# Kernel tuning notes

Hardware: AMD Instinct MI355X
Metric: run time of the kernel (lower is better)

## Reference

```python
import jax, jax.numpy as jnp
import numpy as np

H, C = 4, 128          # heads, hidden_channels
HC = H * C             # 512
F_IN = 9               # node_feat_dim
G_DIM = 50             # global_feat_dim (20 + 30 MACCS)
N = 30000              # nodes
E = 240000             # edges (before self-loops)
B = 64                 # graphs
EPS_BN = 1e-5
SLOPE = 0.2            # GATv2 LeakyReLU negative slope


def _glorot(key, shape):
    fan_in, fan_out = shape[0], shape[-1]
    lim = (6.0 / (fan_in + fan_out)) ** 0.5
    return jax.random.uniform(key, shape, jnp.float32, -lim, lim)


def setup_inputs() -> dict:
    key = jax.random.key(0)
    ks = jax.random.split(key, 20)
    x = jax.random.normal(ks[0], (N, F_IN), jnp.float32)
    global_feat = jax.random.normal(ks[1], (B, G_DIM), jnp.float32)
    edge_index = jax.random.randint(ks[2], (2, E), 0, N, jnp.int64) if jax.config.jax_enable_x64 else jax.random.randint(ks[2], (2, E), 0, N, jnp.int32)
    batch = jnp.sort(jax.random.randint(ks[3], (N,), 0, B, edge_index.dtype))
    return {
        "x": x, "global_feat": global_feat,
        # GATv2 layer 1
        "W1l": _glorot(ks[4], (F_IN, HC)), "b1l": jnp.zeros((HC,), jnp.float32),
        "W1r": _glorot(ks[5], (F_IN, HC)), "b1r": jnp.zeros((HC,), jnp.float32),
        "att1": _glorot(ks[6], (1, H, C))[0], "bias1": jnp.zeros((HC,), jnp.float32),
        # GATv2 layer 2
        "W2l": _glorot(ks[7], (HC, HC)), "b2l": jnp.zeros((HC,), jnp.float32),
        "W2r": _glorot(ks[8], (HC, HC)), "b2r": jnp.zeros((HC,), jnp.float32),
        "att2": _glorot(ks[9], (1, H, C))[0], "bias2": jnp.zeros((HC,), jnp.float32),
        # BatchNorms
        "bn1_g": jnp.ones((HC,), jnp.float32), "bn1_b": jnp.zeros((HC,), jnp.float32),
        "bn2_g": jnp.ones((HC,), jnp.float32), "bn2_b": jnp.zeros((HC,), jnp.float32),
        # MLP head
        "fc1_w": _glorot(ks[10], (HC + G_DIM, C)), "fc1_b": jnp.zeros((C,), jnp.float32),
        "fc2_w": _glorot(ks[11], (C, 1)), "fc2_b": jnp.zeros((1,), jnp.float32),
        "edge_index": edge_index, "batch": batch,
    }


def gatv2_layer(x, src, dst, Wl, bl, Wr, br, att, bias):
    n = x.shape[0]
    xl = (x @ Wl + bl).reshape(n, H, C)   # source transform
    xr = (x @ Wr + br).reshape(n, H, C)   # target transform
    m = xl[src] + xr[dst]                 # [E, H, C] gathered messages
    e = jnp.sum(jax.nn.leaky_relu(m, SLOPE) * att, axis=-1)  # [E, H]
    # segment softmax over edges grouped by target node
    e_max = jax.ops.segment_max(e, dst, num_segments=n)
    p = jnp.exp(e - e_max[dst])
    denom = jax.ops.segment_sum(p, dst, num_segments=n)
    alpha = p / (denom[dst] + 1e-16)      # [E, H]
    out = jax.ops.segment_sum(alpha[:, :, None] * xl[src], dst, num_segments=n)
    return out.reshape(n, HC) + bias


def batchnorm(x, g, b):
    mu = jnp.mean(x, axis=0)
    var = jnp.mean((x - mu) ** 2, axis=0)  # biased var (torch BN train mode)
    return (x - mu) * jax.lax.rsqrt(var + EPS_BN) * g + b


def reference(x, global_feat, W1l, b1l, W1r, b1r, att1, bias1,
              W2l, b2l, W2r, b2r, att2, bias2,
              bn1_g, bn1_b, bn2_g, bn2_b,
              fc1_w, fc1_b, fc2_w, fc2_b, edge_index, batch):
    n = x.shape[0]
    # add self-loops (PyG GATv2 default)
    loops = jnp.arange(n, dtype=edge_index.dtype)
    src = jnp.concatenate([edge_index[0], loops])
    dst = jnp.concatenate([edge_index[1], loops])

    h = gatv2_layer(x, src, dst, W1l, b1l, W1r, b1r, att1, bias1)
    h = jax.nn.relu(batchnorm(h, bn1_g, bn1_b))
    h = gatv2_layer(h, src, dst, W2l, b2l, W2r, b2r, att2, bias2)
    h = jax.nn.relu(batchnorm(h, bn2_g, bn2_b))

    # global mean pool over graphs
    sums = jax.ops.segment_sum(h, batch, num_segments=B)
    counts = jax.ops.segment_sum(jnp.ones((n, 1), h.dtype), batch, num_segments=B)
    pooled = sums / jnp.maximum(counts, 1.0)

    z = jnp.concatenate([pooled, global_feat], axis=1)
    z = jax.nn.relu(z @ fc1_w + fc1_b)  # dropout is identity in eval
    return jnp.squeeze(z @ fc2_w + fc2_b, axis=-1)
```

## Files before the change

### kernel.cpp

```cpp
#include <hip/hip_runtime.h>
#include <math.h>

#define NHEAD 4
#define CCH 128
#define HCD 512
#define SLOPE 0.2f
#define EPS_BN 1e-5f
#define PSPLIT 8

typedef short s8v __attribute__((ext_vector_type(8)));
typedef float f32x4 __attribute__((ext_vector_type(4)));

__device__ __forceinline__ unsigned short f2bf(float f) {
    unsigned int u = __float_as_uint(f);
    return (unsigned short)((u + 0x7FFFu + ((u >> 16) & 1u)) >> 16);
}
__device__ __forceinline__ float bf2f(unsigned short b) {
    return __uint_as_float(((unsigned int)b) << 16);
}

__global__ void lin1_kernel(const float* __restrict__ x,
                            const float* __restrict__ Wl, const float* __restrict__ bl,
                            const float* __restrict__ Wr, const float* __restrict__ br,
                            float* __restrict__ xl, float* __restrict__ xr, int n) {
    int gid = blockIdx.x * blockDim.x + threadIdx.x;
    if (gid >= n * HCD) return;
    int node = gid >> 9;
    int c = gid & (HCD - 1);
    const float* xrow = x + node * 9;
    float a = bl[c], bz = br[c];
#pragma unroll
    for (int k = 0; k < 9; ++k) {
        float xv = xrow[k];
        a  = fmaf(xv, Wl[k * HCD + c], a);
        bz = fmaf(xv, Wr[k * HCD + c], bz);
    }
    xl[gid] = a;
    xr[gid] = bz;
}

__global__ void splitA_kernel(const float* __restrict__ h,
                              const float* __restrict__ scale, const float* __restrict__ shift,
                              unsigned short* __restrict__ Ah, unsigned short* __restrict__ Al,
                              int total4) {
    int gid = blockIdx.x * blockDim.x + threadIdx.x;
    if (gid >= total4) return;
    int c4 = gid & 127;
    float4 v = ((const float4*)h)[gid];
    float4 sc = ((const float4*)scale)[c4];
    float4 sh = ((const float4*)shift)[c4];
    float f0 = fmaxf(fmaf(v.x, sc.x, sh.x), 0.f);
    float f1 = fmaxf(fmaf(v.y, sc.y, sh.y), 0.f);
    float f2 = fmaxf(fmaf(v.z, sc.z, sh.z), 0.f);
    float f3 = fmaxf(fmaf(v.w, sc.w, sh.w), 0.f);
    unsigned short h0 = f2bf(f0), h1 = f2bf(f1), h2 = f2bf(f2), h3 = f2bf(f3);
    short4 hv = make_short4((short)h0, (short)h1, (short)h2, (short)h3);
    short4 lv = make_short4((short)f2bf(f0 - bf2f(h0)), (short)f2bf(f1 - bf2f(h1)),
                            (short)f2bf(f2 - bf2f(h2)), (short)f2bf(f3 - bf2f(h3)));
    ((short4*)Ah)[gid] = hv;
    ((short4*)Al)[gid] = lv;
}

__global__ void splitBT_kernel(const float* __restrict__ Wl, const float* __restrict__ Wr,
                               unsigned short* __restrict__ BThl, unsigned short* __restrict__ BTll,
                               unsigned short* __restrict__ BThr, unsigned short* __restrict__ BTlr) {
    int gid = blockIdx.x * blockDim.x + threadIdx.x;
    int col = gid >> 9;
    int k = gid & 511;
    float vl = Wl[k * HCD + col];
    float vr = Wr[k * HCD + col];
    unsigned short hl = f2bf(vl);
    unsigned short hr = f2bf(vr);
    BThl[gid] = hl; BTll[gid] = f2bf(vl - bf2f(hl));
    BThr[gid] = hr; BTlr[gid] = f2bf(vr - bf2f(hr));
}

__global__ __launch_bounds__(256) void gemm_mfma_kernel(
        const unsigned short* __restrict__ Ah, const unsigned short* __restrict__ Al,
        const unsigned short* __restrict__ BThL, const unsigned short* __restrict__ BTlL,
        const unsigned short* __restrict__ BThR, const unsigned short* __restrict__ BTlR,
        const float* __restrict__ biasl, const float* __restrict__ biasr,
        float* __restrict__ outL, float* __restrict__ outR, int M) {
    __shared__ short sAh[2][4096], sAl[2][4096], sBh[2][4096], sBl[2][4096];
    const int nrt = gridDim.x >> 3;
    const int bphys = blockIdx.x;
    const int l = (bphys & 7) * nrt + (bphys >> 3);
    const int y = l & 7;
    const int row0 = (l >> 3) * 128;
    const unsigned short* BTh = (y < 4) ? BThL : BThR;
    const unsigned short* BTl = (y < 4) ? BTlL : BTlR;
    const float* bias = (y < 4) ? biasl : biasr;
    float* C = (y < 4) ? outL : outR;
    const int col0 = (y & 3) * 128;
    const int tid  = threadIdx.x;
    const int wave = tid >> 6;
    const int lane = tid & 63;
    const int str = tid >> 2;
    const int skb = tid & 3;

    f32x4 acc[4][4];
#pragma unroll
    for (int i = 0; i < 4; ++i)
#pragma unroll
        for (int j = 0; j < 4; ++j) acc[i][j] = (f32x4){0.f, 0.f, 0.f, 0.f};

    const int abase = (wave & 1) * 2048;
    const int bbase = (wave >> 1) * 2048;
    const int rkb = lane >> 4;
    const int rrow = (lane & 15) ^ (rkb << 1);
    const int roff = rkb * 128 + rrow * 8;

    s8v pAh[2], pAl[2], pBh[2], pBl[2];
    const s8v zero8 = (s8v){0,0,0,0,0,0,0,0};

#define GLOAD(k0)                                                                     \
    {                                                                                 \
        _Pragma("unroll")                                                             \
        for (int cc = 0; cc < 2; ++cc) {                                              \
            int r = str + cc * 64;                                                    \
            if (row0 + r < M) {                                                       \
                pAh[cc] = *(const s8v*)(Ah + (size_t)(row0 + r) * 512 + (k0) + skb * 8); \
                pAl[cc] = *(const s8v*)(Al + (size_t)(row0 + r) * 512 + (k0) + skb * 8); \
            } else { pAh[cc] = zero8; pAl[cc] = zero8; }                              \
            pBh[cc] = *(const s8v*)(BTh + (size_t)(col0 + r) * 512 + (k0) + skb * 8); \
            pBl[cc] = *(const s8v*)(BTl + (size_t)(col0 + r) * 512 + (k0) + skb * 8); \
        }                                                                             \
    }

#define LSTORE(buf)                                                                   \
    {                                                                                 \
        _Pragma("unroll")                                                             \
        for (int cc = 0; cc < 2; ++cc) {                                              \
            int r = str + cc * 64;                                                    \
            int idx = (r >> 4) * 512 + skb * 128 + (((r & 15) ^ (skb << 1)) * 8);     \
            *(s8v*)&sAh[buf][idx] = pAh[cc];                                          \
            *(s8v*)&sAl[buf][idx] = pAl[cc];                                          \
            *(s8v*)&sBh[buf][idx] = pBh[cc];                                          \
            *(s8v*)&sBl[buf][idx] = pBl[cc];                                          \
        }                                                                             \
    }

    GLOAD(0);
    LSTORE(0);
    GLOAD(32);
    __syncthreads();

    for (int k0 = 0; k0 < 512; k0 += 32) {
        const int cur = (k0 >> 5) & 1;
#pragma unroll
        for (int sr = 0; sr < 4; ++sr) {
            s8v ah = *(const s8v*)&sAh[cur][abase + sr * 512 + roff];
            s8v al = *(const s8v*)&sAl[cur][abase + sr * 512 + roff];
#pragma unroll
            for (int sc = 0; sc < 4; ++sc) {
                s8v bh = *(const s8v*)&sBh[cur][bbase + sc * 512 + roff];
                s8v bl = *(const s8v*)&sBl[cur][bbase + sc * 512 + roff];
                acc[sr][sc] = __builtin_amdgcn_mfma_f32_16x16x32_bf16(ah, bh, acc[sr][sc], 0, 0, 0);
                acc[sr][sc] = __builtin_amdgcn_mfma_f32_16x16x32_bf16(al, bh, acc[sr][sc], 0, 0, 0);
                acc[sr][sc] = __builtin_amdgcn_mfma_f32_16x16x32_bf16(ah, bl, acc[sr][sc], 0, 0, 0);
            }
        }
        if (k0 + 32 < 512) {
            LSTORE(cur ^ 1);
            if (k0 + 64 < 512) GLOAD(k0 + 64);
            __syncthreads();
        }
    }
#undef GLOAD
#undef LSTORE
    const int crow = row0 + (wave & 1) * 64;
    const int ccol = col0 + (wave >> 1) * 64;
#pragma unroll
    for (int sr = 0; sr < 4; ++sr) {
        int rbase = crow + sr * 16 + ((lane >> 4) << 2);
#pragma unroll
        for (int sc = 0; sc < 4; ++sc) {
            int col = ccol + sc * 16 + (lane & 15);
            float bb = bias[col];
#pragma unroll
            for (int j = 0; j < 4; ++j) {
                int r = rbase + j;
                if (r < M) C[(size_t)r * 512 + col] = acc[sr][sc][j] + bb;
            }
        }
    }
}


__global__ void hist_kernel(const int* __restrict__ edst, int* __restrict__ deg, int E, int Etot) {
    int e = blockIdx.x * blockDim.x + threadIdx.x;
    if (e >= Etot) return;
    int dst = (e < E) ? edst[e] : (e - E);
    atomicAdd(&deg[dst], 1);
}

__global__ __launch_bounds__(1024) void scan_kernel(const int* __restrict__ deg,
                                                    int* __restrict__ rowstart, int n) {
    __shared__ int buf[1024];
    __shared__ int carry;
    if (threadIdx.x == 0) carry = 0;
    __syncthreads();
    for (int base = 0; base < n; base += 1024) {
        int i = base + (int)threadIdx.x;
        int v = (i < n) ? deg[i] : 0;
        buf[threadIdx.x] = v;
        __syncthreads();
        for (int off = 1; off < 1024; off <<= 1) {
            int t = (threadIdx.x >= (unsigned)off) ? buf[threadIdx.x - off] : 0;
            __syncthreads();
            buf[threadIdx.x] += t;
            __syncthreads();
        }
        if (i < n) rowstart[i] = carry + buf[threadIdx.x] - v;
        int blocksum = buf[1023];
        __syncthreads();
        if (threadIdx.x == 0) carry += blocksum;
        __syncthreads();
    }
    if (threadIdx.x == 0) rowstart[n] = carry;
}

__global__ void scatter_kernel(const int* __restrict__ esrc, const int* __restrict__ edst,
                               const int* __restrict__ rowstart, int* __restrict__ cursor,
                               int* __restrict__ s_src, int E, int Etot) {
    int e = blockIdx.x * blockDim.x + threadIdx.x;
    if (e >= Etot) return;
    int src = (e < E) ? esrc[e] : (e - E);
    int dst = (e < E) ? edst[e] : (e - E);
    int pos = rowstart[dst] + atomicAdd(&cursor[dst], 1);
    s_src[pos] = src;
}

__global__ __launch_bounds__(256) void gat_fused_kernel(
        const float* __restrict__ xl, const float* __restrict__ xr,
        const float* __restrict__ att,
        const int* __restrict__ rowstart, const int* __restrict__ s_src,
        float* __restrict__ out) {
    int node = blockIdx.x;
    int h    = threadIdx.x >> 6;
    int lane = threadIdx.x & 63;
    int beg = rowstart[node];
    int end = rowstart[node + 1];
    int c0 = h * CCH + (lane << 1);
    float2 r2 = *(const float2*)(xr + (size_t)node * HCD + c0);
    float2 a2 = *(const float2*)(att + c0);
    float m = -3.0e38f, den = 0.f, acc0 = 0.f, acc1 = 0.f;

    int j = beg;
    float2 q0, q1, q2, q3;
    q0 = *(const float2*)(xl + (size_t)s_src[j] * HCD + c0);
    if (j + 1 < end) q1 = *(const float2*)(xl + (size_t)s_src[j + 1] * HCD + c0);
    if (j + 2 < end) q2 = *(const float2*)(xl + (size_t)s_src[j + 2] * HCD + c0);
    if (j + 3 < end) q3 = *(const float2*)(xl + (size_t)s_src[j + 3] * HCD + c0);

    while (j + 1 < end) {
        float2 A = q0, B = q1;
        q0 = q2; q1 = q3;
        if (j + 4 < end) q2 = *(const float2*)(xl + (size_t)s_src[j + 4] * HCD + c0);
        if (j + 5 < end) q3 = *(const float2*)(xl + (size_t)s_src[j + 5] * HCD + c0);
        float ta0 = A.x + r2.x; ta0 = (ta0 > 0.f) ? ta0 : SLOPE * ta0;
        float ta1 = A.y + r2.y; ta1 = (ta1 > 0.f) ? ta1 : SLOPE * ta1;
        float tb0 = B.x + r2.x; tb0 = (tb0 > 0.f) ? tb0 : SLOPE * tb0;
        float tb1 = B.y + r2.y; tb1 = (tb1 > 0.f) ? tb1 : SLOPE * tb1;
        float sA = fmaf(ta0, a2.x, ta1 * a2.y);
        float sB = fmaf(tb0, a2.x, tb1 * a2.y);
#pragma unroll
        for (int k = 1; k < 64; k <<= 1) {
            sA += __shfl_xor(sA, k);
            sB += __shfl_xor(sB, k);
        }
        float mn = fmaxf(m, fmaxf(sA, sB));
        float sc = expf(m - mn);
        float pA = expf(sA - mn);
        float pB = expf(sB - mn);
        den  = fmaf(den,  sc, pA + pB);
        acc0 = fmaf(acc0, sc, fmaf(pA, A.x, pB * B.x));
        acc1 = fmaf(acc1, sc, fmaf(pA, A.y, pB * B.y));
        m = mn;
        j += 2;
    }
    if (j < end) {
        float2 A = q0;
        float ta0 = A.x + r2.x; ta0 = (ta0 > 0.f) ? ta0 : SLOPE * ta0;
        float ta1 = A.y + r2.y; ta1 = (ta1 > 0.f) ? ta1 : SLOPE * ta1;
        float sA = fmaf(ta0, a2.x, ta1 * a2.y);
#pragma unroll
        for (int k = 1; k < 64; k <<= 1) sA += __shfl_xor(sA, k);
        float mn = fmaxf(m, sA);
        float sc = expf(m - mn);
        float pA = expf(sA - mn);
        den  = fmaf(den,  sc, pA);
        acc0 = fmaf(acc0, sc, pA * A.x);
        acc1 = fmaf(acc1, sc, pA * A.y);
    }
    float inv = 1.0f / (den + 1e-16f);
    *(float2*)(out + (size_t)node * HCD + c0) = make_float2(acc0 * inv, acc1 * inv);
}

__global__ void bn_stats_kernel(const float* __restrict__ h, float* __restrict__ sum,
                                float* __restrict__ sumsq, int n) {
    int c = blockIdx.y * blockDim.x + threadIdx.x;
    int r0 = blockIdx.x * 128;
    int r1 = min(r0 + 128, n);
    float s = 0.f, s2 = 0.f;
    for (int r = r0; r < r1; ++r) {
        float v = h[(size_t)r * HCD + c];
        s += v;
        s2 = fmaf(v, v, s2);
    }
    atomicAdd(&sum[c], s);
    atomicAdd(&sumsq[c], s2);
}

__global__ void bn_finalize_kernel(const float* __restrict__ sum, const float* __restrict__ sumsq,
                                   const float* __restrict__ g, const float* __restrict__ b,
                                   float* __restrict__ scale, float* __restrict__ shift, int n) {
    int c = threadIdx.x;
    float inv_n = 1.0f / (float)n;
    float mu = sum[c] * inv_n;
    float var = fmaxf(sumsq[c] * inv_n - mu * mu, 0.0f);
    float sc = g[c] * rsqrtf(var + EPS_BN);
    scale[c] = sc;
    shift[c] = b[c] - mu * sc;
}

__device__ __forceinline__ int lower_bound_i(const int* __restrict__ a, int n, int key) {
    int lo = 0, hi = n;
    while (lo < hi) {
        int mid = (lo + hi) >> 1;
        if (a[mid] < key) lo = mid + 1; else hi = mid;
    }
    return lo;
}

__global__ void pool_partial_kernel(const float* __restrict__ h, const int* __restrict__ batch,
                                    const float* __restrict__ scale, const float* __restrict__ shift,
                                    float* __restrict__ pooled, int n) {
    int g = blockIdx.x;
    int chunk = blockIdx.y;
    int c = threadIdx.x;
    int start = lower_bound_i(batch, n, g);
    int end   = lower_bound_i(batch, n, g + 1);
    int len = end - start;
    int cs = start + (int)(((long long)len * chunk) / PSPLIT);
    int ce = start + (int)(((long long)len * (chunk + 1)) / PSPLIT);
    if (cs >= ce) return;
    float sc = scale[c], sh = shift[c];
    float s = 0.f;
    for (int r = cs; r < ce; ++r)
        s += fmaxf(fmaf(h[(size_t)r * HCD + c], sc, sh), 0.f);
    atomicAdd(&pooled[(size_t)g * HCD + c], s);
}

__global__ void head_kernel(const float* __restrict__ pooled, const float* __restrict__ gfeat,
                            const int* __restrict__ batch,
                            const float* __restrict__ fc1w, const float* __restrict__ fc1b,
                            const float* __restrict__ fc2w, const float* __restrict__ fc2b,
                            float* __restrict__ out, int gdim, int n) {
    int g = blockIdx.x;
    int j = threadIdx.x;
    int start = lower_bound_i(batch, n, g);
    int end   = lower_bound_i(batch, n, g + 1);
    float icnt = 1.0f / (float)max(end - start, 1);
    float acc = fc1b[j];
    const float* prow = pooled + (size_t)g * HCD;
    for (int i = 0; i < HCD; ++i) acc = fmaf(prow[i] * icnt, fc1w[i * CCH + j], acc);
    const float* grow = gfeat + (size_t)g * gdim;
    for (int i = 0; i < gdim; ++i) acc = fmaf(grow[i], fc1w[(HCD + i) * CCH + j], acc);
    acc = fmaxf(acc, 0.f);
    __shared__ float z[CCH];
    z[j] = acc * fc2w[j];
    __syncthreads();
    for (int s = CCH / 2; s > 0; s >>= 1) {
        if (j < s) z[j] += z[j + s];
        __syncthreads();
    }
    if (j == 0) out[g] = z[0] + fc2b[0];
}

extern "C" void kernel_launch(void* const* d_in, const int* in_sizes, int n_in,
                              void* d_out, int out_size, void* d_ws, size_t ws_size,
                              hipStream_t stream) {
    const float* x     = (const float*)d_in[0];
    const float* gfeat = (const float*)d_in[1];
    const float* W1l   = (const float*)d_in[2];
    const float* b1l   = (const float*)d_in[3];
    const float* W1r   = (const float*)d_in[4];
    const float* b1r   = (const float*)d_in[5];
    const float* att1  = (const float*)d_in[6];
    const float* W2l   = (const float*)d_in[8];
    const float* b2l   = (const float*)d_in[9];
    const float* W2r   = (const float*)d_in[10];
    const float* b2r   = (const float*)d_in[11];
    const float* att2  = (const float*)d_in[12];
    const float* bn1_g = (const float*)d_in[14];
    const float* bn1_b = (const float*)d_in[15];
    const float* bn2_g = (const float*)d_in[16];
    const float* bn2_b = (const float*)d_in[17];
    const float* fc1w  = (const float*)d_in[18];
    const float* fc1b  = (const float*)d_in[19];
    const float* fc2w  = (const float*)d_in[20];
    const float* fc2b  = (const float*)d_in[21];
    const int* eidx    = (const int*)d_in[22];
    const int* batch   = (const int*)d_in[23];

    const int n    = in_sizes[0] / 9;
    const int E    = in_sizes[22] / 2;
    const int Etot = E + n;
    const int b    = out_size;
    const int gdim = in_sizes[1] / b;
    const int* esrc = eidx;
    const int* edst = eidx + E;

    float* ws = (float*)d_ws;
    size_t nHC = (size_t)n * HCD;
    float* xl      = ws;
    float* xr      = xl + nHC;
    float* hbuf    = xr + nHC;
    int* deg       = (int*)(hbuf + nHC);
    int* rowstart  = deg + n;
    int* cursor    = rowstart + n + 1;
    int* s_src     = cursor + n;
    float* bnsum   = (float*)(s_src + Etot);
    float* bnsumsq = bnsum + HCD;
    float* bnscale = bnsumsq + HCD;
    float* bnshift = bnscale + HCD;
    float* pooled  = bnshift + HCD;
    unsigned short* Ah   = (unsigned short*)(pooled + (size_t)b * HCD);
    unsigned short* Al   = Ah + nHC;
    unsigned short* BThl = Al + nHC;
    unsigned short* BTll = BThl + HCD * HCD;
    unsigned short* BThr = BTll + HCD * HCD;
    unsigned short* BTlr = BThr + HCD * HCD;

    const int BLK = 256;
    const int linBlocks  = (int)((nHC + BLK - 1) / BLK);
    const int eBlocks    = (Etot + BLK - 1) / BLK;
    const int bnxBlocks  = (n + 127) / 128;
    const int saBlocks   = (int)((nHC / 4 + BLK - 1) / BLK);
    const int nrt        = (n + 127) / 128;
    dim3 gemmGrid(nrt * 8);

    hipMemsetAsync(deg, 0, (size_t)(2 * n + 1) * sizeof(int), stream);
    hipMemsetAsync(cursor, 0, (size_t)n * sizeof(int), stream);
    hist_kernel<<<eBlocks, BLK, 0, stream>>>(edst, deg, E, Etot);
    scan_kernel<<<1, 1024, 0, stream>>>(deg, rowstart, n);
    scatter_kernel<<<eBlocks, BLK, 0, stream>>>(esrc, edst, rowstart, cursor, s_src, E, Etot);
    splitBT_kernel<<<(HCD * HCD) / BLK, BLK, 0, stream>>>(W2l, W2r, BThl, BTll, BThr, BTlr);

    lin1_kernel<<<linBlocks, BLK, 0, stream>>>(x, W1l, b1l, W1r, b1r, xl, xr, n);
    gat_fused_kernel<<<n, 256, 0, stream>>>(xl, xr, att1, rowstart, s_src, hbuf);
    hipMemsetAsync(bnsum, 0, HCD * 2 * sizeof(float), stream);
    bn_stats_kernel<<<dim3(bnxBlocks, 2), BLK, 0, stream>>>(hbuf, bnsum, bnsumsq, n);
    bn_finalize_kernel<<<1, HCD, 0, stream>>>(bnsum, bnsumsq, bn1_g, bn1_b, bnscale, bnshift, n);

    splitA_kernel<<<saBlocks, BLK, 0, stream>>>(hbuf, bnscale, bnshift, Ah, Al, (int)(nHC / 4));
    gemm_mfma_kernel<<<gemmGrid, BLK, 0, stream>>>(Ah, Al, BThl, BTll, BThr, BTlr,
                                                   b2l, b2r, xl, xr, n);
    gat_fused_kernel<<<n, 256, 0, stream>>>(xl, xr, att2, rowstart, s_src, hbuf);
    hipMemsetAsync(bnsum, 0, HCD * 2 * sizeof(float), stream);
    bn_stats_kernel<<<dim3(bnxBlocks, 2), BLK, 0, stream>>>(hbuf, bnsum, bnsumsq, n);
    bn_finalize_kernel<<<1, HCD, 0, stream>>>(bnsum, bnsumsq, bn2_g, bn2_b, bnscale, bnshift, n);

    hipMemsetAsync(pooled, 0, (size_t)b * HCD * sizeof(float), stream);
    pool_partial_kernel<<<dim3(b, PSPLIT), HCD, 0, stream>>>(hbuf, batch, bnscale, bnshift, pooled, n);
    head_kernel<<<b, CCH, 0, stream>>>(pooled, gfeat, batch, fc1w, fc1b, fc2w, fc2b,
                                       (float*)d_out, gdim, n);
}
```

Baseline: 775.8 us.

## Parallelize CSR scan across blocks and map one wavefront per GAT node

```diff
diff --git a/kernel.cpp b/kernel.cpp
--- a/kernel.cpp
+++ b/kernel.cpp
@@ -194,30 +194,43 @@
     atomicAdd(&deg[dst], 1);
 }
 
-__global__ __launch_bounds__(1024) void scan_kernel(const int* __restrict__ deg,
-                                                    int* __restrict__ rowstart, int n) {
+__global__ void scan1_kernel(const int* __restrict__ deg, int* __restrict__ rowstart,
+                             int* __restrict__ bsum, int n) {
+    __shared__ int buf[256];
+    int i = blockIdx.x * 256 + (int)threadIdx.x;
+    int v = (i < n) ? deg[i] : 0;
+    buf[threadIdx.x] = v;
+    __syncthreads();
+    for (int off = 1; off < 256; off <<= 1) {
+        int t = (threadIdx.x >= (unsigned)off) ? buf[threadIdx.x - off] : 0;
+        __syncthreads();
+        buf[threadIdx.x] += t;
+        __syncthreads();
+    }
+    if (i < n) rowstart[i] = buf[threadIdx.x] - v;
+    if (threadIdx.x == 255) bsum[blockIdx.x] = buf[255];
+}
+
+__global__ __launch_bounds__(1024) void scan2_kernel(int* __restrict__ bsum,
+                                                     int* __restrict__ boff,
+                                                     int nb, int* __restrict__ total_out) {
     __shared__ int buf[1024];
-    __shared__ int carry;
-    if (threadIdx.x == 0) carry = 0;
+    int v = ((int)threadIdx.x < nb) ? bsum[threadIdx.x] : 0;
+    buf[threadIdx.x] = v;
     __syncthreads();
-    for (int base = 0; base < n; base += 1024) {
-        int i = base + (int)threadIdx.x;
-        int v = (i < n) ? deg[i] : 0;
-        buf[threadIdx.x] = v;
+    for (int off = 1; off < 1024; off <<= 1) {
+        int t = (threadIdx.x >= (unsigned)off) ? buf[threadIdx.x - off] : 0;
         __syncthreads();
-        for (int off = 1; off < 1024; off <<= 1) {
-            int t = (threadIdx.x >= (unsigned)off) ? buf[threadIdx.x - off] : 0;
-            __syncthreads();
-            buf[threadIdx.x] += t;
-            __syncthreads();
-        }
-        if (i < n) rowstart[i] = carry + buf[threadIdx.x] - v;
-        int blocksum = buf[1023];
+        buf[threadIdx.x] += t;
         __syncthreads();
-        if (threadIdx.x == 0) carry += blocksum;
-        __syncthreads();
-    }
-    if (threadIdx.x == 0) rowstart[n] = carry;
+    }
+    if ((int)threadIdx.x < nb) boff[threadIdx.x] = buf[threadIdx.x] - v;
+    if (threadIdx.x == 1023) *total_out = buf[1023];
+}
+
+__global__ void scan3_kernel(int* __restrict__ rowstart, const int* __restrict__ boff, int n) {
+    int i = blockIdx.x * 256 + (int)threadIdx.x;
+    if (i < n) rowstart[i] += boff[blockIdx.x];
 }
 
 __global__ void scatter_kernel(const int* __restrict__ esrc, const int* __restrict__ edst,
@@ -235,37 +248,70 @@
         const float* __restrict__ xl, const float* __restrict__ xr,
         const float* __restrict__ att,
         const int* __restrict__ rowstart, const int* __restrict__ s_src,
-        float* __restrict__ out) {
-    int node = blockIdx.x;
-    int h    = threadIdx.x >> 6;
+        float* __restrict__ out, int n) {
+    int node = blockIdx.x * 4 + (int)(threadIdx.x >> 6);
+    if (node >= n) return;
     int lane = threadIdx.x & 63;
+    int c0 = lane << 3;
+    const float4* xr4 = (const float4*)(xr + (size_t)node * HCD + c0);
+    float4 r0 = xr4[0], r1 = xr4[1];
+    const float4* at4 = (const float4*)(att + c0);
+    float4 a0 = at4[0], a1 = at4[1];
     int beg = rowstart[node];
     int end = rowstart[node + 1];
-    int c0 = h * CCH + (lane << 1);
-    float2 r2 = *(const float2*)(xr + (size_t)node * HCD + c0);
-    float2 a2 = *(const float2*)(att + c0);
-    float m = -3.0e38f, den = 0.f, acc0 = 0.f, acc1 = 0.f;
+    float m = -3.0e38f, den = 0.f;
+    float4 acc0 = make_float4(0.f, 0.f, 0.f, 0.f);
+    float4 acc1 = make_float4(0.f, 0.f, 0.f, 0.f);
+
+#define SCORE(s, X0, X1)                                                       \
+    {                                                                          \
+        float t;                                                               \
+        s = 0.f;                                                               \
+        t = X0.x + r0.x; t = (t > 0.f) ? t : SLOPE * t; s = fmaf(t, a0.x, s);  \
+        t = X0.y + r0.y; t = (t > 0.f) ? t : SLOPE * t; s = fmaf(t, a0.y, s);  \
+        t = X0.z + r0.z; t = (t > 0.f) ? t : SLOPE * t; s = fmaf(t, a0.z, s);  \
+        t = X0.w + r0.w; t = (t > 0.f) ? t : SLOPE * t; s = fmaf(t, a0.w, s);  \
+        t = X1.x + r1.x; t = (t > 0.f) ? t : SLOPE * t; s = fmaf(t, a1.x, s);  \
+        t = X1.y + r1.y; t = (t > 0.f) ? t : SLOPE * t; s = fmaf(t, a1.y, s);  \
+        t = X1.z + r1.z; t = (t > 0.f) ? t : SLOPE * t; s = fmaf(t, a1.z, s);  \
+        t = X1.w + r1.w; t = (t > 0.f) ? t : SLOPE * t; s = fmaf(t, a1.w, s);  \
+    }
 
     int j = beg;
-    float2 q0, q1, q2, q3;
-    q0 = *(const float2*)(xl + (size_t)s_src[j] * HCD + c0);
-    if (j + 1 < end) q1 = *(const float2*)(xl + (size_t)s_src[j + 1] * HCD + c0);
-    if (j + 2 < end) q2 = *(const float2*)(xl + (size_t)s_src[j + 2] * HCD + c0);
-    if (j + 3 < end) q3 = *(const float2*)(xl + (size_t)s_src[j + 3] * HCD + c0);
+    float4 qa0, qa1, qb0, qb1, qc0, qc1, qd0, qd1;
+    {
+        const float4* p = (const float4*)(xl + (size_t)s_src[j] * HCD + c0);
+        qa0 = p[0]; qa1 = p[1];
+    }
+    if (j + 1 < end) {
+        const float4* p = (const float4*)(xl + (size_t)s_src[j + 1] * HCD + c0);
+        qb0 = p[0]; qb1 = p[1];
+    }
+    if (j + 2 < end) {
+        const float4* p = (const float4*)(xl + (size_t)s_src[j + 2] * HCD + c0);
+        qc0 = p[0]; qc1 = p[1];
+    }
+    if (j + 3 < end) {
+        const float4* p = (const float4*)(xl + (size_t)s_src[j + 3] * HCD + c0);
+        qd0 = p[0]; qd1 = p[1];
+    }
 
     while (j + 1 < end) {
-        float2 A = q0, B = q1;
-        q0 = q2; q1 = q3;
-        if (j + 4 < end) q2 = *(const float2*)(xl + (size_t)s_src[j + 4] * HCD + c0);
-        if (j + 5 < end) q3 = *(const float2*)(xl + (size_t)s_src[j + 5] * HCD + c0);
-        float ta0 = A.x + r2.x; ta0 = (ta0 > 0.f) ? ta0 : SLOPE * ta0;
-        float ta1 = A.y + r2.y; ta1 = (ta1 > 0.f) ? ta1 : SLOPE * ta1;
-        float tb0 = B.x + r2.x; tb0 = (tb0 > 0.f) ? tb0 : SLOPE * tb0;
-        float tb1 = B.y + r2.y; tb1 = (tb1 > 0.f) ? tb1 : SLOPE * tb1;
-        float sA = fmaf(ta0, a2.x, ta1 * a2.y);
-        float sB = fmaf(tb0, a2.x, tb1 * a2.y);
-#pragma unroll
-        for (int k = 1; k < 64; k <<= 1) {
+        float4 A0 = qa0, A1 = qa1, B0 = qb0, B1 = qb1;
+        qa0 = qc0; qa1 = qc1; qb0 = qd0; qb1 = qd1;
+        if (j + 4 < end) {
+            const float4* p = (const float4*)(xl + (size_t)s_src[j + 4] * HCD + c0);
+            qc0 = p[0]; qc1 = p[1];
+        }
+        if (j + 5 < end) {
+            const float4* p = (const float4*)(xl + (size_t)s_src[j + 5] * HCD + c0);
+            qd0 = p[0]; qd1 = p[1];
+        }
+        float sA, sB;
+        SCORE(sA, A0, A1);
+        SCORE(sB, B0, B1);
+#pragma unroll
+        for (int k = 1; k < 16; k <<= 1) {
             sA += __shfl_xor(sA, k);
             sB += __shfl_xor(sB, k);
         }
@@ -273,28 +319,42 @@
         float sc = expf(m - mn);
         float pA = expf(sA - mn);
         float pB = expf(sB - mn);
-        den  = fmaf(den,  sc, pA + pB);
-        acc0 = fmaf(acc0, sc, fmaf(pA, A.x, pB * B.x));
-        acc1 = fmaf(acc1, sc, fmaf(pA, A.y, pB * B.y));
+        den = fmaf(den, sc, pA + pB);
+        acc0.x = fmaf(acc0.x, sc, fmaf(pA, A0.x, pB * B0.x));
+        acc0.y = fmaf(acc0.y, sc, fmaf(pA, A0.y, pB * B0.y));
+        acc0.z = fmaf(acc0.z, sc, fmaf(pA, A0.z, pB * B0.z));
+        acc0.w = fmaf(acc0.w, sc, fmaf(pA, A0.w, pB * B0.w));
+        acc1.x = fmaf(acc1.x, sc, fmaf(pA, A1.x, pB * B1.x));
+        acc1.y = fmaf(acc1.y, sc, fmaf(pA, A1.y, pB * B1.y));
+        acc1.z = fmaf(acc1.z, sc, fmaf(pA, A1.z, pB * B1.z));
+        acc1.w = fmaf(acc1.w, sc, fmaf(pA, A1.w, pB * B1.w));
         m = mn;
         j += 2;
     }
     if (j < end) {
-        float2 A = q0;
-        float ta0 = A.x + r2.x; ta0 = (ta0 > 0.f) ? ta0 : SLOPE * ta0;
-        float ta1 = A.y + r2.y; ta1 = (ta1 > 0.f) ? ta1 : SLOPE * ta1;
-        float sA = fmaf(ta0, a2.x, ta1 * a2.y);
-#pragma unroll
-        for (int k = 1; k < 64; k <<= 1) sA += __shfl_xor(sA, k);
+        float4 A0 = qa0, A1 = qa1;
+        float sA;
+        SCORE(sA, A0, A1);
+#pragma unroll
+        for (int k = 1; k < 16; k <<= 1) sA += __shfl_xor(sA, k);
         float mn = fmaxf(m, sA);
         float sc = expf(m - mn);
         float pA = expf(sA - mn);
-        den  = fmaf(den,  sc, pA);
-        acc0 = fmaf(acc0, sc, pA * A.x);
-        acc1 = fmaf(acc1, sc, pA * A.y);
-    }
+        den = fmaf(den, sc, pA);
+        acc0.x = fmaf(acc0.x, sc, pA * A0.x);
+        acc0.y = fmaf(acc0.y, sc, pA * A0.y);
+        acc0.z = fmaf(acc0.z, sc, pA * A0.z);
+        acc0.w = fmaf(acc0.w, sc, pA * A0.w);
+        acc1.x = fmaf(acc1.x, sc, pA * A1.x);
+        acc1.y = fmaf(acc1.y, sc, pA * A1.y);
+        acc1.z = fmaf(acc1.z, sc, pA * A1.z);
+        acc1.w = fmaf(acc1.w, sc, pA * A1.w);
+    }
+#undef SCORE
     float inv = 1.0f / (den + 1e-16f);
-    *(float2*)(out + (size_t)node * HCD + c0) = make_float2(acc0 * inv, acc1 * inv);
+    float4* o = (float4*)(out + (size_t)node * HCD + c0);
+    o[0] = make_float4(acc0.x * inv, acc0.y * inv, acc0.z * inv, acc0.w * inv);
+    o[1] = make_float4(acc1.x * inv, acc1.y * inv, acc1.z * inv, acc1.w * inv);
 }
 
 __global__ void bn_stats_kernel(const float* __restrict__ h, float* __restrict__ sum,
@@ -420,7 +480,9 @@
     int* deg       = (int*)(hbuf + nHC);
     int* rowstart  = deg + n;
     int* cursor    = rowstart + n + 1;
-    int* s_src     = cursor + n;
+    int* bsum      = cursor + n;
+    int* boff      = bsum + 1024;
+    int* s_src     = boff + 1024;
     float* bnsum   = (float*)(s_src + Etot);
     float* bnsumsq = bnsum + HCD;
     float* bnscale = bnsumsq + HCD;
@@ -439,17 +501,21 @@
     const int bnxBlocks  = (n + 127) / 128;
     const int saBlocks   = (int)((nHC / 4 + BLK - 1) / BLK);
     const int nrt        = (n + 127) / 128;
+    const int scBlocks   = (n + 255) / 256;
+    const int gatBlocks  = (n + 3) / 4;
     dim3 gemmGrid(nrt * 8);
 
     hipMemsetAsync(deg, 0, (size_t)(2 * n + 1) * sizeof(int), stream);
     hipMemsetAsync(cursor, 0, (size_t)n * sizeof(int), stream);
     hist_kernel<<<eBlocks, BLK, 0, stream>>>(edst, deg, E, Etot);
-    scan_kernel<<<1, 1024, 0, stream>>>(deg, rowstart, n);
+    scan1_kernel<<<scBlocks, 256, 0, stream>>>(deg, rowstart, bsum, n);
+    scan2_kernel<<<1, 1024, 0, stream>>>(bsum, boff, scBlocks, rowstart + n);
+    scan3_kernel<<<scBlocks, 256, 0, stream>>>(rowstart, boff, n);
     scatter_kernel<<<eBlocks, BLK, 0, stream>>>(esrc, edst, rowstart, cursor, s_src, E, Etot);
     splitBT_kernel<<<(HCD * HCD) / BLK, BLK, 0, stream>>>(W2l, W2r, BThl, BTll, BThr, BTlr);
 
     lin1_kernel<<<linBlocks, BLK, 0, stream>>>(x, W1l, b1l, W1r, b1r, xl, xr, n);
-    gat_fused_kernel<<<n, 256, 0, stream>>>(xl, xr, att1, rowstart, s_src, hbuf);
+    gat_fused_kernel<<<gatBlocks, 256, 0, stream>>>(xl, xr, att1, rowstart, s_src, hbuf, n);
     hipMemsetAsync(bnsum, 0, HCD * 2 * sizeof(float), stream);
     bn_stats_kernel<<<dim3(bnxBlocks, 2), BLK, 0, stream>>>(hbuf, bnsum, bnsumsq, n);
     bn_finalize_kernel<<<1, HCD, 0, stream>>>(bnsum, bnsumsq, bn1_g, bn1_b, bnscale, bnshift, n);
@@ -457,7 +523,7 @@
     splitA_kernel<<<saBlocks, BLK, 0, stream>>>(hbuf, bnscale, bnshift, Ah, Al, (int)(nHC / 4));
     gemm_mfma_kernel<<<gemmGrid, BLK, 0, stream>>>(Ah, Al, BThl, BTll, BThr, BTlr,
                                                    b2l, b2r, xl, xr, n);
-    gat_fused_kernel<<<n, 256, 0, stream>>>(xl, xr, att2, rowstart, s_src, hbuf);
+    gat_fused_kernel<<<gatBlocks, 256, 0, stream>>>(xl, xr, att2, rowstart, s_src, hbuf, n);
     hipMemsetAsync(bnsum, 0, HCD * 2 * sizeof(float), stream);
     bn_stats_kernel<<<dim3(bnxBlocks, 2), BLK, 0, stream>>>(hbuf, bnsum, bnsumsq, n);
     bn_finalize_kernel<<<1, HCD, 0, stream>>>(bnsum, bnsumsq, bn2_g, bn2_b, bnscale, bnshift, n);
```

Result: faster. 713.5 us (-8.0%).
